# Performance work log

Measured on AMD Instinct MI355X. Metric: run time of the kernel, lower is better.

Reference implementation:

```python
import jax, jax.numpy as jnp
import numpy as np

N_QUBITS = 12
K_STEPS = 6
VOCAB = 32000
D_EMB = 512
N_CLASSES = 8
B = 256
SEQ = 128
DIM = 2 ** N_QUBITS


def apply_1q(psi, U, q):
    # psi: [B, 2^n]; U: [2,2] (shared) or [B,2,2] (per-sample). Apply on wire q
    # (PennyLane convention: wire 0 = most significant axis).
    b = psi.shape[0]
    left, right = 2 ** q, 2 ** (N_QUBITS - q - 1)
    st = psi.reshape(b, left, 2, right)
    if U.ndim == 3:
        st = jnp.einsum('bij,bajr->bair', U, st)
    else:
        st = jnp.einsum('ij,bajr->bair', U, st)
    return st.reshape(b, DIM)


def apply_cnot(psi, c, t):
    b = psi.shape[0]
    st = psi.reshape((b,) + (2,) * N_QUBITS)
    c_ax, t_ax = 1 + c, 1 + t
    c0 = jnp.take(st, 0, axis=c_ax)
    c1 = jnp.take(st, 1, axis=c_ax)
    t_ax2 = t_ax - 1 if t_ax > c_ax else t_ax  # axis shift after take
    c1 = jnp.flip(c1, axis=t_ax2)
    return jnp.stack([c0, c1], axis=c_ax).reshape(b, DIM)


def ry_mat(angle):
    # angle: [B] -> [B,2,2] complex64
    c = jnp.cos(angle / 2)
    s = jnp.sin(angle / 2)
    row0 = jnp.stack([c, -s], axis=-1)
    row1 = jnp.stack([s, c], axis=-1)
    return jnp.stack([row0, row1], axis=-2).astype(jnp.complex64)


def rot_mat(phi, theta, omega):
    # PennyLane Rot(phi, theta, omega) = RZ(omega) RY(theta) RZ(phi)
    c = jnp.cos(theta / 2)
    s = jnp.sin(theta / 2)
    ep = jnp.exp(-0.5j * (phi + omega).astype(jnp.complex64))
    em = jnp.exp(0.5j * (phi - omega).astype(jnp.complex64))
    m = jnp.stack([jnp.stack([ep * c, -em * s]), jnp.stack([jnp.conj(em) * s, jnp.conj(ep) * c])])
    return m.astype(jnp.complex64)


def block(psi, x, theta_k):
    # data reupload RY(x_i), trainable Rot, ring of CNOTs (noiseless)
    for i in range(N_QUBITS):
        psi = apply_1q(psi, ry_mat(x[:, i]), i)
    for i in range(N_QUBITS):
        psi = apply_1q(psi, rot_mat(theta_k[i, 0], theta_k[i, 1], theta_k[i, 2]), i)
    for i in range(N_QUBITS - 1):
        psi = apply_cnot(psi, i, i + 1)
    psi = apply_cnot(psi, N_QUBITS - 1, 0)
    return psi


def z_expvals(psi):
    # <Z_i> for all wires from |psi|^2
    b = psi.shape[0]
    p = (psi.real ** 2 + psi.imag ** 2).reshape((b,) + (2,) * N_QUBITS)
    zs = []
    for i in range(N_QUBITS):
        axes = tuple(ax for ax in range(1, N_QUBITS + 1) if ax != 1 + i)
        m = p.sum(axis=axes)  # [B,2]
        zs.append(m[:, 0] - m[:, 1])
    return jnp.stack(zs, axis=-1)  # [B, n_qubits]


def _forward(input_ids, attention_mask, emb_table, proj_w, proj_b, theta, head_w, head_b):
    # encoder: embed -> masked mean pool -> tanh(linear) * pi
    e = emb_table[input_ids]                              # [B,S,D]
    mask = attention_mask[:, :, None].astype(jnp.float32)
    pooled = (e * mask).sum(axis=1) / jnp.clip(mask.sum(axis=1), 1.0)
    x = jnp.tanh(pooled @ proj_w.T + proj_b) * jnp.float32(np.pi)  # [B, n_qubits]

    b = x.shape[0]
    psi = jnp.zeros((b, DIM), jnp.complex64).at[:, 0].set(1.0)
    readouts = []
    for k in range(K_STEPS):
        psi = block(psi, x, theta[k])
        readouts.append(z_expvals(psi))
    step_readouts = jnp.stack(readouts, axis=0)           # [K,B,n_qubits]
    step_logits = step_readouts @ head_w.T + head_b       # [K,B,n_classes]
    return step_logits, step_readouts, step_logits[-1]


def setup_inputs() -> dict:
    key = jax.random.key(0)
    ks = jax.random.split(key, 6)
    input_ids = jax.random.randint(ks[0], (B, SEQ), 0, VOCAB)
    attention_mask = jnp.ones((B, SEQ), dtype=jnp.int32)
    emb_table = jax.random.normal(ks[1], (VOCAB, D_EMB), jnp.float32)
    emb_table = emb_table.at[0].set(0.0)  # padding_idx=0 row is zeros
    proj_w = jax.random.normal(ks[2], (N_QUBITS, D_EMB), jnp.float32) / np.sqrt(D_EMB)
    proj_b = jnp.zeros((N_QUBITS,), jnp.float32)
    theta = 0.01 * jax.random.normal(ks[3], (K_STEPS, N_QUBITS, 3), jnp.float32)
    head_w = jax.random.normal(ks[4], (N_CLASSES, N_QUBITS), jnp.float32) / np.sqrt(N_QUBITS)
    head_b = jnp.zeros((N_CLASSES,), jnp.float32)
    return {'input_ids': input_ids, 'attention_mask': attention_mask,
            'emb_table': emb_table, 'proj_w': proj_w, 'proj_b': proj_b,
            'theta': theta, 'head_w': head_w, 'head_b': head_b}


def reference(input_ids, attention_mask, emb_table, proj_w, proj_b, theta, head_w, head_b):
    return _forward(input_ids, attention_mask, emb_table, proj_w, proj_b, theta, head_w, head_b)
```

## Files before the change

kernel.cpp:

```cpp
#include <hip/hip_runtime.h>
#include <math.h>

#define NQ 12
#define DIM 4096
#define KS 6
#define BB 256
#define SEQ 128
#define DEMB 512


#define REG_GATE(P, W) { \
    float4 c0 = *(const float4*)&s_u[k][W][0]; \
    float4 c1 = *(const float4*)&s_u[k][W][4]; \
    float u00r=c0.x,u00i=c0.y,u01r=c0.z,u01i=c0.w; \
    float u10r=c1.x,u10i=c1.y,u11r=c1.z,u11i=c1.w; \
    _Pragma("unroll") \
    for (int r0 = 0; r0 < 8; ++r0) if (!(r0 & (1 << (P)))) { \
        int r1 = r0 | (1 << (P)); \
        float2 A = a[r0], Bv = a[r1]; \
        a[r0].x = u00r*A.x - u00i*A.y + u01r*Bv.x - u01i*Bv.y; \
        a[r0].y = u00r*A.y + u00i*A.x + u01r*Bv.y + u01i*Bv.x; \
        a[r1].x = u10r*A.x - u10i*A.y + u11r*Bv.x - u11i*Bv.y; \
        a[r1].y = u10r*A.y + u10i*A.x + u11r*Bv.y + u11i*Bv.x; \
    } }

#define BF_PLAIN(v, m) { float p_ = __shfl_xor(v, m, 64); v = v + p_; }
#define BF_SIGN(v, m)  { float p_ = __shfl_xor(v, m, 64); float d_ = v - p_; \
                         v = (lane & m) ? -d_ : d_; }

#define WAVE_FENCE() asm volatile("s_waitcnt lgkmcnt(0)" ::: "memory")

__device__ __forceinline__ int swz14(int x) { return x ^ ((x >> 4) & 14); }

__global__ __launch_bounds__(512) void fused_kernel(
    const int* __restrict__ ids, const int* __restrict__ mask,
    const float* __restrict__ emb, const float* __restrict__ pw,
    const float* __restrict__ pb, const float* __restrict__ theta,
    const float* __restrict__ hw, const float* __restrict__ hb,
    float* __restrict__ readouts, float* __restrict__ logits,
    float* __restrict__ last)
{
    __shared__ __align__(16) float2 buf0[DIM];
    __shared__ __align__(16) float2 buf1[DIM];
    __shared__ __align__(16) float  s_u[KS][NQ][8];
    __shared__ float  s_red[8][NQ];
    __shared__ float  s_msum[4];
    __shared__ float  s_wred[2][NQ];
    __shared__ float  s_x[NQ];
    __shared__ float  s_hw[8 * NQ];
    __shared__ float  s_hb[8];

    int b = blockIdx.x;
    int tid = threadIdx.x;
    int lane = tid & 63, wave = tid >> 6;

    int*   s_ids = (int*)buf1;
    float* s_m   = (float*)buf1 + SEQ;
    float4* s_part = (float4*)buf0;

    if (tid < SEQ) {
        s_ids[tid] = ids[b * SEQ + tid];
        s_m[tid]   = (float)mask[b * SEQ + tid];
    }
    if (tid >= 256 && tid < 256 + 8 * NQ) s_hw[tid - 256] = hw[tid - 256];
    if (tid >= 384 && tid < 392)          s_hb[tid - 384] = hb[tid - 384];
    __syncthreads();

    {
        int g = tid >> 7, e = tid & 127;
        float4 acc = make_float4(0.f, 0.f, 0.f, 0.f);
        float msum = 0.f;
        #pragma unroll 4
        for (int s = g; s < SEQ; s += 4) {
            float m = s_m[s];
            float4 v = ((const float4*)emb)[(size_t)s_ids[s] * 128 + e];
            acc.x = fmaf(m, v.x, acc.x);
            acc.y = fmaf(m, v.y, acc.y);
            acc.z = fmaf(m, v.z, acc.z);
            acc.w = fmaf(m, v.w, acc.w);
            msum += m;
        }
        __syncthreads();
        s_part[g * 128 + e] = acc;
        if (e == 0) s_msum[g] = msum;
    }
    __syncthreads();

    if (tid < 128) {
        float tm = fmaxf(s_msum[0] + s_msum[1] + s_msum[2] + s_msum[3], 1.f);
        float inv = 1.f / tm;
        float4 p0 = s_part[0 * 128 + tid], p1 = s_part[1 * 128 + tid];
        float4 p2 = s_part[2 * 128 + tid], p3 = s_part[3 * 128 + tid];
        float4 p;
        p.x = (p0.x + p1.x + p2.x + p3.x) * inv;
        p.y = (p0.y + p1.y + p2.y + p3.y) * inv;
        p.z = (p0.z + p1.z + p2.z + p3.z) * inv;
        p.w = (p0.w + p1.w + p2.w + p3.w) * inv;
        float z[NQ];
        #pragma unroll
        for (int i = 0; i < NQ; ++i) {
            float4 w4 = ((const float4*)pw)[i * 128 + tid];
            z[i] = p.x * w4.x + p.y * w4.y + p.z * w4.z + p.w * w4.w;
        }
        #pragma unroll
        for (int i = 0; i < NQ; ++i) {
            #pragma unroll
            for (int off = 32; off > 0; off >>= 1)
                z[i] += __shfl_xor(z[i], off, 64);
        }
        if ((tid & 63) == 0) {
            int w = tid >> 6;
            #pragma unroll
            for (int i = 0; i < NQ; ++i) s_wred[w][i] = z[i];
        }
    }
    __syncthreads();
    if (tid < NQ) {
        float d = pb[tid] + s_wred[0][tid] + s_wred[1][tid];
        s_x[tid] = tanhf(d) * 3.14159274101257324f;
    }
    __syncthreads();

    if (tid < KS * NQ) {
        int k = tid / NQ, w = tid % NQ;
        float ang = s_x[w];
        float cy = cosf(0.5f * ang), sy = sinf(0.5f * ang);
        const float* th = theta + (k * NQ + w) * 3;
        float phi = th[0], te = th[1], om = th[2];
        float ct = cosf(0.5f * te), st = sinf(0.5f * te);
        float a1 = -0.5f * (phi + om);
        float epr = cosf(a1), epi = sinf(a1);
        float a2 = 0.5f * (phi - om);
        float emr = cosf(a2), emi = sinf(a2);
        float R00r = epr * ct,  R00i = epi * ct;
        float R01r = -emr * st, R01i = -emi * st;
        float R10r = emr * st,  R10i = -emi * st;
        float R11r = epr * ct,  R11i = -epi * ct;
        s_u[k][w][0] =  R00r * cy + R01r * sy;
        s_u[k][w][1] =  R00i * cy + R01i * sy;
        s_u[k][w][2] = -R00r * sy + R01r * cy;
        s_u[k][w][3] = -R00i * sy + R01i * cy;
        s_u[k][w][4] =  R10r * cy + R11r * sy;
        s_u[k][w][5] =  R10i * cy + R11i * sy;
        s_u[k][w][6] = -R10r * sy + R11r * cy;
        s_u[k][w][7] = -R10i * sy + R11i * cy;
    }

    int T8 = tid << 3;
    int baseA  = swz14(T8);
    int baseA4 = baseA >> 1;
    int addrB[8], addrC[8], addrD[8], idxP[8];
    #pragma unroll
    for (int r = 0; r < 8; ++r) {
        addrB[r] = swz14((lane & 7) + 8 * r + 64 * (lane >> 3) + 512 * wave);
        addrC[r] = swz14(lane + 64 * r + 512 * wave);
        int jD   = lane + 64 * wave + 512 * r;
        addrD[r] = swz14(jD);
        int b0 = (jD >> 11) & 1;
        int pref = b0, outv = 0;
        for (int w = 1; w < NQ; ++w) {
            pref ^= (jD >> (11 - w)) & 1;
            outv |= pref << (11 - w);
        }
        outv |= (b0 ^ pref) << 11;
        idxP[r] = swz14(outv);
    }
    int w0b = wave & 1, w1b = (wave >> 1) & 1, w2b = (wave >> 2) & 1;
    int wall = w0b ^ w1b ^ w2b;

    float2 a[8];
    #pragma unroll
    for (int r = 0; r < 8; ++r) a[r] = make_float2(0.f, 0.f);
    if (tid == 0) a[0].x = 1.f;
    __syncthreads();

    for (int k = 0; k < KS; ++k) {
        REG_GATE(0, 11) REG_GATE(1, 10) REG_GATE(2, 9)

        #pragma unroll
        for (int i = 0; i < 4; ++i)
            ((float4*)buf0)[baseA4 ^ i] =
                make_float4(a[2*i].x, a[2*i].y, a[2*i+1].x, a[2*i+1].y);
        WAVE_FENCE();
        #pragma unroll
        for (int r = 0; r < 8; ++r) a[r] = buf0[addrB[r]];

        REG_GATE(0, 8) REG_GATE(1, 7) REG_GATE(2, 6)

        #pragma unroll
        for (int r = 0; r < 8; ++r) buf0[addrB[r]] = a[r];
        WAVE_FENCE();
        #pragma unroll
        for (int r = 0; r < 8; ++r) a[r] = buf0[addrC[r]];

        REG_GATE(0, 5) REG_GATE(1, 4) REG_GATE(2, 3)

        #pragma unroll
        for (int r = 0; r < 8; ++r) buf0[addrC[r]] = a[r];
        __syncthreads();
        #pragma unroll
        for (int r = 0; r < 8; ++r) a[r] = buf0[addrD[r]];

        REG_GATE(0, 2) REG_GATE(1, 1) REG_GATE(2, 0)

        #pragma unroll
        for (int r = 0; r < 8; ++r) buf1[idxP[r]] = a[r];

        {
            float p[8];
            #pragma unroll
            for (int r = 0; r < 8; ++r)
                p[r] = a[r].x * a[r].x + a[r].y * a[r].y;
            float Q1 = (p[0]+p[1]+p[6]+p[7]) - (p[2]+p[3]+p[4]+p[5]);
            float Q2 = (p[0]+p[3]+p[5]+p[6]) - (p[1]+p[2]+p[4]+p[7]);
            float Q0 = (p[0]+p[3]+p[4]+p[7]) - (p[1]+p[2]+p[5]+p[6]);
            float q1 = Q1, q2p = Q2, q0 = Q0;
            BF_PLAIN(q1,32) BF_PLAIN(q1,16) BF_PLAIN(q1,8)
            BF_PLAIN(q1,4)  BF_PLAIN(q1,2)  BF_PLAIN(q1,1)
            BF_PLAIN(q2p,32) BF_PLAIN(q2p,16) BF_PLAIN(q2p,8)
            BF_PLAIN(q2p,4)  BF_PLAIN(q2p,2)  BF_PLAIN(q2p,1)
            BF_SIGN(q0,32) BF_SIGN(q0,16) BF_SIGN(q0,8)
            BF_SIGN(q0,4)  BF_SIGN(q0,2)  BF_SIGN(q0,1)
            float c = Q2;
            BF_SIGN(c,32);
            float w6v = c; BF_PLAIN(w6v,16) BF_PLAIN(w6v,8) BF_PLAIN(w6v,4)
                           BF_PLAIN(w6v,2)  BF_PLAIN(w6v,1)
            BF_SIGN(c,16);
            float w7v = c; BF_PLAIN(w7v,8) BF_PLAIN(w7v,4)
                           BF_PLAIN(w7v,2) BF_PLAIN(w7v,1)
            BF_SIGN(c,8);
            float w8v = c; BF_PLAIN(w8v,4) BF_PLAIN(w8v,2) BF_PLAIN(w8v,1)
            BF_SIGN(c,4);
            float w9v = c; BF_PLAIN(w9v,2) BF_PLAIN(w9v,1)
            BF_SIGN(c,2);
            float w10v = c; BF_PLAIN(w10v,1)
            BF_SIGN(c,1);
            if (lane == 0) {
                float* sr = s_red[wave];
                sr[0]  = wall ? -q0  : q0;
                sr[1]  = q1;
                sr[2]  = q2p;
                sr[3]  = w2b ? -q2p : q2p;
                sr[4]  = (w1b ^ w2b) ? -q2p : q2p;
                sr[5]  = wall ? -q2p : q2p;
                sr[6]  = wall ? -w6v : w6v;
                sr[7]  = wall ? -w7v : w7v;
                sr[8]  = wall ? -w8v : w8v;
                sr[9]  = wall ? -w9v : w9v;
                sr[10] = wall ? -w10v : w10v;
                sr[11] = wall ? -c   : c;
            }
        }

        __syncthreads();
        #pragma unroll
        for (int i = 0; i < 4; ++i) {
            float4 v = ((float4*)buf1)[baseA4 ^ i];
            a[2*i]   = make_float2(v.x, v.y);
            a[2*i+1] = make_float2(v.z, v.w);
        }

        if (tid < NQ) {
            float s = 0.f;
            #pragma unroll
            for (int w2 = 0; w2 < 8; ++w2) s += s_red[w2][tid];
            readouts[(k * BB + b) * NQ + tid] = s;
        }
        if (tid < 8) {
            float acc2 = s_hb[tid];
            #pragma unroll
            for (int i = 0; i < NQ; ++i) {
                float si = 0.f;
                #pragma unroll
                for (int w2 = 0; w2 < 8; ++w2) si += s_red[w2][i];
                acc2 = fmaf(si, s_hw[tid * NQ + i], acc2);
            }
            logits[(k * BB + b) * 8 + tid] = acc2;
            if (k == KS - 1) last[b * 8 + tid] = acc2;
        }
    }
}

extern "C" void kernel_launch(void* const* d_in, const int* in_sizes, int n_in,
                              void* d_out, int out_size, void* d_ws, size_t ws_size,
                              hipStream_t stream) {
    const int*   ids   = (const int*)d_in[0];
    const int*   mask  = (const int*)d_in[1];
    const float* emb   = (const float*)d_in[2];
    const float* pw    = (const float*)d_in[3];
    const float* pb    = (const float*)d_in[4];
    const float* theta = (const float*)d_in[5];
    const float* hw    = (const float*)d_in[6];
    const float* hb    = (const float*)d_in[7];
    float* out = (float*)d_out;

    float* readouts = out + KS * BB * 8;
    float* last     = out + KS * BB * 8 + KS * BB * NQ;

    fused_kernel<<<BB, 512, 0, stream>>>(ids, mask, emb, pw, pb, theta,
                                         hw, hb, readouts, out, last);
}
```

Before: 139.9 us.

## Double block size to 1024 threads with 4 amplitudes per thread

```diff
diff --git a/kernel.cpp b/kernel.cpp
--- a/kernel.cpp
+++ b/kernel.cpp
@@ -9,13 +9,13 @@
 #define DEMB 512
 
 
-#define REG_GATE(P, W) { \
+#define RG(P, W) { \
     float4 c0 = *(const float4*)&s_u[k][W][0]; \
     float4 c1 = *(const float4*)&s_u[k][W][4]; \
     float u00r=c0.x,u00i=c0.y,u01r=c0.z,u01i=c0.w; \
     float u10r=c1.x,u10i=c1.y,u11r=c1.z,u11i=c1.w; \
     _Pragma("unroll") \
-    for (int r0 = 0; r0 < 8; ++r0) if (!(r0 & (1 << (P)))) { \
+    for (int r0 = 0; r0 < 4; ++r0) if (!(r0 & (1 << (P)))) { \
         int r1 = r0 | (1 << (P)); \
         float2 A = a[r0], Bv = a[r1]; \
         a[r0].x = u00r*A.x - u00i*A.y + u01r*Bv.x - u01i*Bv.y; \
@@ -32,7 +32,7 @@
 
 __device__ __forceinline__ int swz14(int x) { return x ^ ((x >> 4) & 14); }
 
-__global__ __launch_bounds__(512) void fused_kernel(
+__global__ __launch_bounds__(1024) void fused_kernel(
     const int* __restrict__ ids, const int* __restrict__ mask,
     const float* __restrict__ emb, const float* __restrict__ pw,
     const float* __restrict__ pb, const float* __restrict__ theta,
@@ -42,9 +42,10 @@
 {
     __shared__ __align__(16) float2 buf0[DIM];
     __shared__ __align__(16) float2 buf1[DIM];
+    __shared__ __align__(16) float2 buf2[DIM];
     __shared__ __align__(16) float  s_u[KS][NQ][8];
-    __shared__ float  s_red[8][NQ];
-    __shared__ float  s_msum[4];
+    __shared__ float  s_red[16][NQ];
+    __shared__ float  s_msum[8];
     __shared__ float  s_wred[2][NQ];
     __shared__ float  s_x[NQ];
     __shared__ float  s_hw[8 * NQ];
@@ -71,7 +72,7 @@
         float4 acc = make_float4(0.f, 0.f, 0.f, 0.f);
         float msum = 0.f;
         #pragma unroll 4
-        for (int s = g; s < SEQ; s += 4) {
+        for (int s = g; s < SEQ; s += 8) {
             float m = s_m[s];
             float4 v = ((const float4*)emb)[(size_t)s_ids[s] * 128 + e];
             acc.x = fmaf(m, v.x, acc.x);
@@ -87,15 +88,17 @@
     __syncthreads();
 
     if (tid < 128) {
-        float tm = fmaxf(s_msum[0] + s_msum[1] + s_msum[2] + s_msum[3], 1.f);
+        float tm = s_msum[0] + s_msum[1] + s_msum[2] + s_msum[3]
+                 + s_msum[4] + s_msum[5] + s_msum[6] + s_msum[7];
+        tm = fmaxf(tm, 1.f);
         float inv = 1.f / tm;
-        float4 p0 = s_part[0 * 128 + tid], p1 = s_part[1 * 128 + tid];
-        float4 p2 = s_part[2 * 128 + tid], p3 = s_part[3 * 128 + tid];
-        float4 p;
-        p.x = (p0.x + p1.x + p2.x + p3.x) * inv;
-        p.y = (p0.y + p1.y + p2.y + p3.y) * inv;
-        p.z = (p0.z + p1.z + p2.z + p3.z) * inv;
-        p.w = (p0.w + p1.w + p2.w + p3.w) * inv;
+        float4 p = make_float4(0.f, 0.f, 0.f, 0.f);
+        #pragma unroll
+        for (int g = 0; g < 8; ++g) {
+            float4 pg = s_part[g * 128 + tid];
+            p.x += pg.x; p.y += pg.y; p.z += pg.z; p.w += pg.w;
+        }
+        p.x *= inv; p.y *= inv; p.z *= inv; p.w *= inv;
         float z[NQ];
         #pragma unroll
         for (int i = 0; i < NQ; ++i) {
@@ -146,88 +149,104 @@
         s_u[k][w][7] = -R10i * sy + R11i * cy;
     }
 
-    int T8 = tid << 3;
-    int baseA  = swz14(T8);
-    int baseA4 = baseA >> 1;
-    int addrB[8], addrC[8], addrD[8], idxP[8];
+    int T4 = tid << 2;
+    int bA4 = swz14(T4) >> 1;
+    int aB[4], aC[4], aD[4], aE[4], aF[4], idxP[4];
     #pragma unroll
-    for (int r = 0; r < 8; ++r) {
-        addrB[r] = swz14((lane & 7) + 8 * r + 64 * (lane >> 3) + 512 * wave);
-        addrC[r] = swz14(lane + 64 * r + 512 * wave);
-        int jD   = lane + 64 * wave + 512 * r;
-        addrD[r] = swz14(jD);
-        int b0 = (jD >> 11) & 1;
+    for (int r = 0; r < 4; ++r) {
+        aB[r] = swz14((wave << 8) | ((lane >> 2) << 4) | (r << 2) | (lane & 3));
+        aC[r] = swz14((wave << 8) | ((lane >> 4) << 6) | (r << 4) | (lane & 15));
+        aD[r] = swz14((wave << 8) | (r << 6) | lane);
+        aE[r] = swz14(((lane >> 4) << 10) | (r << 8) | (wave << 4) | (lane & 15));
+        int jF = (r << 10) | ((lane >> 4) << 8) | (wave << 4) | (lane & 15);
+        aF[r] = swz14(jF);
+        int b0 = (jF >> 11) & 1;
         int pref = b0, outv = 0;
         for (int w = 1; w < NQ; ++w) {
-            pref ^= (jD >> (11 - w)) & 1;
+            pref ^= (jF >> (11 - w)) & 1;
             outv |= pref << (11 - w);
         }
         outv |= (b0 ^ pref) << 11;
         idxP[r] = swz14(outv);
     }
-    int w0b = wave & 1, w1b = (wave >> 1) & 1, w2b = (wave >> 2) & 1;
-    int wall = w0b ^ w1b ^ w2b;
-
-    float2 a[8];
+    int s3v   = (wave >> 3) & 1;
+    int s32v  = s3v ^ ((wave >> 2) & 1);
+    int s321v = s32v ^ ((wave >> 1) & 1);
+    int sallv = s321v ^ (wave & 1);
+
+    float2 a[4];
     #pragma unroll
-    for (int r = 0; r < 8; ++r) a[r] = make_float2(0.f, 0.f);
+    for (int r = 0; r < 4; ++r) a[r] = make_float2(0.f, 0.f);
     if (tid == 0) a[0].x = 1.f;
     __syncthreads();
 
     for (int k = 0; k < KS; ++k) {
-        REG_GATE(0, 11) REG_GATE(1, 10) REG_GATE(2, 9)
-
-        #pragma unroll
-        for (int i = 0; i < 4; ++i)
-            ((float4*)buf0)[baseA4 ^ i] =
+        RG(0, 11) RG(1, 10)
+
+        #pragma unroll
+        for (int i = 0; i < 2; ++i)
+            ((float4*)buf0)[bA4 ^ i] =
                 make_float4(a[2*i].x, a[2*i].y, a[2*i+1].x, a[2*i+1].y);
         WAVE_FENCE();
         #pragma unroll
-        for (int r = 0; r < 8; ++r) a[r] = buf0[addrB[r]];
-
-        REG_GATE(0, 8) REG_GATE(1, 7) REG_GATE(2, 6)
-
-        #pragma unroll
-        for (int r = 0; r < 8; ++r) buf0[addrB[r]] = a[r];
+        for (int r = 0; r < 4; ++r) a[r] = buf0[aB[r]];
+
+        RG(0, 9) RG(1, 8)
+
+        #pragma unroll
+        for (int r = 0; r < 4; ++r) buf0[aB[r]] = a[r];
         WAVE_FENCE();
         #pragma unroll
-        for (int r = 0; r < 8; ++r) a[r] = buf0[addrC[r]];
-
-        REG_GATE(0, 5) REG_GATE(1, 4) REG_GATE(2, 3)
-
-        #pragma unroll
-        for (int r = 0; r < 8; ++r) buf0[addrC[r]] = a[r];
+        for (int r = 0; r < 4; ++r) a[r] = buf0[aC[r]];
+
+        RG(0, 7) RG(1, 6)
+
+        #pragma unroll
+        for (int r = 0; r < 4; ++r) buf0[aC[r]] = a[r];
+        WAVE_FENCE();
+        #pragma unroll
+        for (int r = 0; r < 4; ++r) a[r] = buf0[aD[r]];
+
+        RG(0, 5) RG(1, 4)
+
+        #pragma unroll
+        for (int r = 0; r < 4; ++r) buf0[aD[r]] = a[r];
         __syncthreads();
         #pragma unroll
-        for (int r = 0; r < 8; ++r) a[r] = buf0[addrD[r]];
-
-        REG_GATE(0, 2) REG_GATE(1, 1) REG_GATE(2, 0)
-
-        #pragma unroll
-        for (int r = 0; r < 8; ++r) buf1[idxP[r]] = a[r];
+        for (int r = 0; r < 4; ++r) a[r] = buf0[aE[r]];
+
+        RG(0, 3) RG(1, 2)
+
+        #pragma unroll
+        for (int r = 0; r < 4; ++r) buf1[aE[r]] = a[r];
+        WAVE_FENCE();
+        #pragma unroll
+        for (int r = 0; r < 4; ++r) a[r] = buf1[aF[r]];
+
+        RG(0, 1) RG(1, 0)
+
+        #pragma unroll
+        for (int r = 0; r < 4; ++r) buf2[idxP[r]] = a[r];
 
         {
-            float p[8];
-            #pragma unroll
-            for (int r = 0; r < 8; ++r)
-                p[r] = a[r].x * a[r].x + a[r].y * a[r].y;
-            float Q1 = (p[0]+p[1]+p[6]+p[7]) - (p[2]+p[3]+p[4]+p[5]);
-            float Q2 = (p[0]+p[3]+p[5]+p[6]) - (p[1]+p[2]+p[4]+p[7]);
-            float Q0 = (p[0]+p[3]+p[4]+p[7]) - (p[1]+p[2]+p[5]+p[6]);
-            float q1 = Q1, q2p = Q2, q0 = Q0;
-            BF_PLAIN(q1,32) BF_PLAIN(q1,16) BF_PLAIN(q1,8)
-            BF_PLAIN(q1,4)  BF_PLAIN(q1,2)  BF_PLAIN(q1,1)
-            BF_PLAIN(q2p,32) BF_PLAIN(q2p,16) BF_PLAIN(q2p,8)
-            BF_PLAIN(q2p,4)  BF_PLAIN(q2p,2)  BF_PLAIN(q2p,1)
-            BF_SIGN(q0,32) BF_SIGN(q0,16) BF_SIGN(q0,8)
-            BF_SIGN(q0,4)  BF_SIGN(q0,2)  BF_SIGN(q0,1)
-            float c = Q2;
+            float p0 = a[0].x*a[0].x + a[0].y*a[0].y;
+            float p1 = a[1].x*a[1].x + a[1].y*a[1].y;
+            float p2 = a[2].x*a[2].x + a[2].y*a[2].y;
+            float p3 = a[3].x*a[3].x + a[3].y*a[3].y;
+            float T1v = (p0 + p3) - (p1 + p2);
+            float T0v = (p0 + p2) - (p1 + p3);
+
+            float v1 = T1v;
+            BF_PLAIN(v1,32) BF_PLAIN(v1,16) BF_PLAIN(v1,8)
+            BF_PLAIN(v1,4)  BF_PLAIN(v1,2)  BF_PLAIN(v1,1)
+
+            float c = T1v;
             BF_SIGN(c,32);
-            float w6v = c; BF_PLAIN(w6v,16) BF_PLAIN(w6v,8) BF_PLAIN(w6v,4)
-                           BF_PLAIN(w6v,2)  BF_PLAIN(w6v,1)
+            float w2v = c; BF_PLAIN(w2v,16) BF_PLAIN(w2v,8) BF_PLAIN(w2v,4)
+                           BF_PLAIN(w2v,2)  BF_PLAIN(w2v,1)
             BF_SIGN(c,16);
-            float w7v = c; BF_PLAIN(w7v,8) BF_PLAIN(w7v,4)
-                           BF_PLAIN(w7v,2) BF_PLAIN(w7v,1)
+            float w3v = c; BF_PLAIN(w3v,8) BF_PLAIN(w3v,4)
+                           BF_PLAIN(w3v,2) BF_PLAIN(w3v,1)
             BF_SIGN(c,8);
             float w8v = c; BF_PLAIN(w8v,4) BF_PLAIN(w8v,2) BF_PLAIN(w8v,1)
             BF_SIGN(c,4);
@@ -235,27 +254,32 @@
             BF_SIGN(c,2);
             float w10v = c; BF_PLAIN(w10v,1)
             BF_SIGN(c,1);
+
+            float q0 = T0v;
+            BF_SIGN(q0,32) BF_SIGN(q0,16) BF_SIGN(q0,8)
+            BF_SIGN(q0,4)  BF_SIGN(q0,2)  BF_SIGN(q0,1)
+
             if (lane == 0) {
                 float* sr = s_red[wave];
-                sr[0]  = wall ? -q0  : q0;
-                sr[1]  = q1;
-                sr[2]  = q2p;
-                sr[3]  = w2b ? -q2p : q2p;
-                sr[4]  = (w1b ^ w2b) ? -q2p : q2p;
-                sr[5]  = wall ? -q2p : q2p;
-                sr[6]  = wall ? -w6v : w6v;
-                sr[7]  = wall ? -w7v : w7v;
-                sr[8]  = wall ? -w8v : w8v;
-                sr[9]  = wall ? -w9v : w9v;
-                sr[10] = wall ? -w10v : w10v;
-                sr[11] = wall ? -c   : c;
+                sr[0]  = sallv ? -q0   : q0;
+                sr[1]  = v1;
+                sr[2]  = w2v;
+                sr[3]  = w3v;
+                sr[4]  = s3v   ? -w3v  : w3v;
+                sr[5]  = s32v  ? -w3v  : w3v;
+                sr[6]  = s321v ? -w3v  : w3v;
+                sr[7]  = sallv ? -w3v  : w3v;
+                sr[8]  = sallv ? -w8v  : w8v;
+                sr[9]  = sallv ? -w9v  : w9v;
+                sr[10] = sallv ? -w10v : w10v;
+                sr[11] = sallv ? -c    : c;
             }
         }
 
         __syncthreads();
         #pragma unroll
-        for (int i = 0; i < 4; ++i) {
-            float4 v = ((float4*)buf1)[baseA4 ^ i];
+        for (int i = 0; i < 2; ++i) {
+            float4 v = ((float4*)buf2)[bA4 ^ i];
             a[2*i]   = make_float2(v.x, v.y);
             a[2*i+1] = make_float2(v.z, v.w);
         }
@@ -263,7 +287,7 @@
         if (tid < NQ) {
             float s = 0.f;
             #pragma unroll
-            for (int w2 = 0; w2 < 8; ++w2) s += s_red[w2][tid];
+            for (int w2 = 0; w2 < 16; ++w2) s += s_red[w2][tid];
             readouts[(k * BB + b) * NQ + tid] = s;
         }
         if (tid < 8) {
@@ -272,7 +296,7 @@
             for (int i = 0; i < NQ; ++i) {
                 float si = 0.f;
                 #pragma unroll
-                for (int w2 = 0; w2 < 8; ++w2) si += s_red[w2][i];
+                for (int w2 = 0; w2 < 16; ++w2) si += s_red[w2][i];
                 acc2 = fmaf(si, s_hw[tid * NQ + i], acc2);
             }
             logits[(k * BB + b) * 8 + tid] = acc2;
@@ -297,6 +321,6 @@
     float* readouts = out + KS * BB * 8;
     float* last     = out + KS * BB * 8 + KS * BB * NQ;
 
-    fused_kernel<<<BB, 512, 0, stream>>>(ids, mask, emb, pw, pb, theta,
-                                         hw, hb, readouts, out, last);
+    fused_kernel<<<BB, 1024, 0, stream>>>(ids, mask, emb, pw, pb, theta,
+                                          hw, hb, readouts, out, last);
 }
```

Measured after the change: 143.9 us. +2.9%, slower.

## Replace intra-wave LDS transposes with shuffle-based butterfly swaps; parallelize gate matrix setup

Applied to the files above, without the earlier changes.

```diff
diff --git a/kernel.cpp b/kernel.cpp
--- a/kernel.cpp
+++ b/kernel.cpp
@@ -9,7 +9,7 @@
 #define DEMB 512
 
 
-#define REG_GATE(P, W) { \
+#define RG(P, W) { \
     float4 c0 = *(const float4*)&s_u[k][W][0]; \
     float4 c1 = *(const float4*)&s_u[k][W][4]; \
     float u00r=c0.x,u00i=c0.y,u01r=c0.z,u01i=c0.w; \
@@ -24,11 +24,18 @@
         a[r1].y = u10r*A.y + u10i*A.x + u11r*Bv.y + u11i*Bv.x; \
     } }
 
+#define SWAPB(lo, hi, M) { \
+    float tx_ = (lane & M) ? lo.x : hi.x; \
+    float ty_ = (lane & M) ? lo.y : hi.y; \
+    tx_ = __shfl_xor(tx_, M, 64); \
+    ty_ = __shfl_xor(ty_, M, 64); \
+    if (lane & M) { lo.x = tx_; lo.y = ty_; } \
+    else          { hi.x = tx_; hi.y = ty_; } \
+}
+
 #define BF_PLAIN(v, m) { float p_ = __shfl_xor(v, m, 64); v = v + p_; }
 #define BF_SIGN(v, m)  { float p_ = __shfl_xor(v, m, 64); float d_ = v - p_; \
                          v = (lane & m) ? -d_ : d_; }
-
-#define WAVE_FENCE() asm volatile("s_waitcnt lgkmcnt(0)" ::: "memory")
 
 __device__ __forceinline__ int swz14(int x) { return x ^ ((x >> 4) & 14); }
 
@@ -121,38 +128,32 @@
     }
     __syncthreads();
 
-    if (tid < KS * NQ) {
-        int k = tid / NQ, w = tid % NQ;
+    if (tid < KS * NQ * 4) {
+        int k = tid / 48;
+        int rem = tid - k * 48;
+        int w = rem >> 2, q = rem & 3;
         float ang = s_x[w];
         float cy = cosf(0.5f * ang), sy = sinf(0.5f * ang);
         const float* th = theta + (k * NQ + w) * 3;
         float phi = th[0], te = th[1], om = th[2];
         float ct = cosf(0.5f * te), st = sinf(0.5f * te);
         float a1 = -0.5f * (phi + om);
-        float epr = cosf(a1), epi = sinf(a1);
-        float a2 = 0.5f * (phi - om);
-        float emr = cosf(a2), emi = sinf(a2);
-        float R00r = epr * ct,  R00i = epi * ct;
-        float R01r = -emr * st, R01i = -emi * st;
-        float R10r = emr * st,  R10i = -emi * st;
-        float R11r = epr * ct,  R11i = -epi * ct;
-        s_u[k][w][0] =  R00r * cy + R01r * sy;
-        s_u[k][w][1] =  R00i * cy + R01i * sy;
-        s_u[k][w][2] = -R00r * sy + R01r * cy;
-        s_u[k][w][3] = -R00i * sy + R01i * cy;
-        s_u[k][w][4] =  R10r * cy + R11r * sy;
-        s_u[k][w][5] =  R10i * cy + R11i * sy;
-        s_u[k][w][6] = -R10r * sy + R11r * cy;
-        s_u[k][w][7] = -R10i * sy + R11i * cy;
+        float a2 =  0.5f * (phi - om);
+        float ar =  cosf(a1) * ct, ai =  sinf(a1) * ct;
+        float br = -cosf(a2) * st, bi = -sinf(a2) * st;
+        float x1 = (q & 1) ? ai : ar;
+        float x2 = (q & 1) ? bi : br;
+        float E  = (q & 2) ? (x2 * cy - x1 * sy) : (x1 * cy + x2 * sy);
+        s_u[k][w][q] = E;
+        s_u[k][w][(q & 2) ? q + 2 : q + 6] = (q == 1 || q == 2) ? -E : E;
     }
 
     int T8 = tid << 3;
     int baseA  = swz14(T8);
     int baseA4 = baseA >> 1;
-    int addrB[8], addrC[8], addrD[8], idxP[8];
+    int addrC[8], addrD[8], idxP[8];
     #pragma unroll
     for (int r = 0; r < 8; ++r) {
-        addrB[r] = swz14((lane & 7) + 8 * r + 64 * (lane >> 3) + 512 * wave);
         addrC[r] = swz14(lane + 64 * r + 512 * wave);
         int jD   = lane + 64 * wave + 512 * r;
         addrD[r] = swz14(jD);
@@ -175,25 +176,25 @@
     __syncthreads();
 
     for (int k = 0; k < KS; ++k) {
-        REG_GATE(0, 11) REG_GATE(1, 10) REG_GATE(2, 9)
-
-        #pragma unroll
-        for (int i = 0; i < 4; ++i)
-            ((float4*)buf0)[baseA4 ^ i] =
-                make_float4(a[2*i].x, a[2*i].y, a[2*i+1].x, a[2*i+1].y);
-        WAVE_FENCE();
-        #pragma unroll
-        for (int r = 0; r < 8; ++r) a[r] = buf0[addrB[r]];
-
-        REG_GATE(0, 8) REG_GATE(1, 7) REG_GATE(2, 6)
-
-        #pragma unroll
-        for (int r = 0; r < 8; ++r) buf0[addrB[r]] = a[r];
-        WAVE_FENCE();
-        #pragma unroll
-        for (int r = 0; r < 8; ++r) a[r] = buf0[addrC[r]];
-
-        REG_GATE(0, 5) REG_GATE(1, 4) REG_GATE(2, 3)
+        RG(0, 11) RG(1, 10) RG(2, 9)
+
+        SWAPB(a[0], a[1], 1) SWAPB(a[2], a[3], 1)
+        SWAPB(a[4], a[5], 1) SWAPB(a[6], a[7], 1)
+        SWAPB(a[0], a[2], 2) SWAPB(a[1], a[3], 2)
+        SWAPB(a[4], a[6], 2) SWAPB(a[5], a[7], 2)
+        SWAPB(a[0], a[4], 4) SWAPB(a[1], a[5], 4)
+        SWAPB(a[2], a[6], 4) SWAPB(a[3], a[7], 4)
+
+        RG(0, 8) RG(1, 7) RG(2, 6)
+
+        SWAPB(a[0], a[1], 8)  SWAPB(a[2], a[3], 8)
+        SWAPB(a[4], a[5], 8)  SWAPB(a[6], a[7], 8)
+        SWAPB(a[0], a[2], 16) SWAPB(a[1], a[3], 16)
+        SWAPB(a[4], a[6], 16) SWAPB(a[5], a[7], 16)
+        SWAPB(a[0], a[4], 32) SWAPB(a[1], a[5], 32)
+        SWAPB(a[2], a[6], 32) SWAPB(a[3], a[7], 32)
+
+        RG(0, 5) RG(1, 4) RG(2, 3)
 
         #pragma unroll
         for (int r = 0; r < 8; ++r) buf0[addrC[r]] = a[r];
@@ -201,7 +202,7 @@
         #pragma unroll
         for (int r = 0; r < 8; ++r) a[r] = buf0[addrD[r]];
 
-        REG_GATE(0, 2) REG_GATE(1, 1) REG_GATE(2, 0)
+        RG(0, 2) RG(1, 1) RG(2, 0)
 
         #pragma unroll
         for (int r = 0; r < 8; ++r) buf1[idxP[r]] = a[r];
```

Measured after the change: 141.7 us. About the same (+1.3%).
